# Optimization experiments

Measured on AMD Instinct MI355X. Metric: run time of the kernel, lower is better.

The kernel has to match this reference:

```python
import jax, jax.numpy as jnp
import numpy as np
from jax import lax

EPS = 1e-12  # torch F.normalize eps

DIM = 192
HEADS = 8
B, H, W = 4, 256, 256


def setup_inputs() -> dict:
    key = jax.random.key(0)
    k1, k2, k3, k4 = jax.random.split(key, 4)
    x = jax.random.normal(k1, (B, DIM, H, W), dtype=jnp.float32)
    # 1x1 conv weights stored as [out, in] matrices (kernel size 1)
    qkv_w = jax.random.normal(k2, (DIM * 3, DIM), dtype=jnp.float32) * (1.0 / np.sqrt(DIM))
    # depthwise 3x3 conv, groups = 3*DIM -> OIHW with I=1
    dw_w = jax.random.normal(k3, (DIM * 3, 1, 3, 3), dtype=jnp.float32) * (1.0 / 3.0)
    proj_w = jax.random.normal(k4, (DIM, DIM), dtype=jnp.float32) * (1.0 / np.sqrt(DIM))
    temperature = jnp.ones((HEADS, 1, 1), dtype=jnp.float32)
    return {"x": x, "qkv_w": qkv_w, "dw_w": dw_w, "proj_w": proj_w, "temperature": temperature}


def _l2_normalize(t):
    # matches torch F.normalize(dim=-1): x / max(||x||, eps)
    n = jnp.sqrt(jnp.sum(t * t, axis=-1, keepdims=True))
    return t / jnp.maximum(n, EPS)


def reference(x, qkv_w, dw_w, proj_w, temperature):
    b, c, h, w = x.shape
    heads = temperature.shape[0]
    head_dim = c // heads
    hw = h * w
    # 1x1 conv == per-pixel GEMM
    qkv = jnp.einsum('bchw,oc->bohw', x, qkv_w)
    # depthwise 3x3 conv, padding=1
    qkv = lax.conv_general_dilated(
        qkv, dw_w, window_strides=(1, 1), padding='SAME',
        dimension_numbers=('NCHW', 'OIHW', 'NCHW'),
        feature_group_count=c * 3)
    q, k, v = jnp.split(qkv, 3, axis=1)
    q = _l2_normalize(q.reshape(b, heads, head_dim, hw))
    k = _l2_normalize(k.reshape(b, heads, head_dim, hw))
    v = v.reshape(b, heads, head_dim, hw)
    # tiny [head_dim, head_dim] attention matrix per (b, head)
    attn = jnp.einsum('bhdn,bhen->bhde', q, k) * temperature  # (heads,1,1) broadcasts
    attn = jax.nn.softmax(attn, axis=-1)
    out = jnp.einsum('bhde,bhen->bhdn', attn, v).reshape(b, c, h, w)
    return jnp.einsum('bchw,oc->bohw', out, proj_w)
```

## Files before the change

### kernel.cpp

```cpp
#include <hip/hip_runtime.h>
#include <stdint.h>

typedef unsigned short u16;
typedef short s16x8 __attribute__((ext_vector_type(8)));
typedef float f32x4 __attribute__((ext_vector_type(4)));

#define HW 65536
#define CD 192
#define C3 576
#define QB ((size_t)HW * C3)

static __device__ __forceinline__ float bf2f(u16 u) {
    return __uint_as_float(((uint32_t)u) << 16);
}
static __device__ __forceinline__ u16 f2bf(float f) {
    uint32_t x = __float_as_uint(f);
    return (u16)((x + 0x7fffu + ((x >> 16) & 1u)) >> 16);
}

__launch_bounds__(256)
__global__ void k_convert(const float* __restrict__ in, u16* __restrict__ out, int n4)
{
    int i = blockIdx.x * 256 + threadIdx.x;
    if (i >= n4) return;
    float4 v = ((const float4*)in)[i];
    ushort4 o;
    o.x = f2bf(v.x); o.y = f2bf(v.y); o.z = f2bf(v.z); o.w = f2bf(v.w);
    ((ushort4*)out)[i] = o;
}

__launch_bounds__(256, 2)
__global__ void k_qkv(const u16* __restrict__ A, const float* __restrict__ x,
                      u16* __restrict__ O, int b0)
{
    __shared__ __attribute__((aligned(16))) u16 As[192 * 40];
    __shared__ __attribute__((aligned(16))) u16 Xs[128 * 40];
    const int t    = threadIdx.x;
    const int pb   = blockIdx.z;
    const int m0g  = blockIdx.y * 192;
    const int p0   = blockIdx.x * 128;
    const int lane = t & 63, wid = t >> 6;
    const int quad = lane >> 4, l16 = lane & 15;
    const int wm0  = (wid >> 1) * 96, wn0 = (wid & 1) * 64;

    f32x4 acc[6][4];
    #pragma unroll
    for (int i = 0; i < 6; i++)
        #pragma unroll
        for (int j = 0; j < 4; j++) acc[i][j] = f32x4{0.f, 0.f, 0.f, 0.f};

    const float* Xb = x + (size_t)(b0 + pb) * CD * HW;

    for (int kk = 0; kk < 6; kk++) {
        if (kk) __syncthreads();
        #pragma unroll
        for (int i = 0; i < 3; i++) {
            int s = t + i * 256;
            int m = s >> 2, part = s & 3;
            uint4 v = *(const uint4*)(A + (size_t)(m0g + m) * CD + kk * 32 + part * 8);
            *(uint4*)(&As[m * 40 + part * 8]) = v;
        }
        #pragma unroll
        for (int i = 0; i < 4; i++) {
            int s = t + i * 256;
            int c_l = s >> 5, seg = s & 31;
            float4 v = *(const float4*)(Xb + (size_t)(kk * 32 + c_l) * HW + p0 + seg * 4);
            Xs[(seg * 4 + 0) * 40 + c_l] = f2bf(v.x);
            Xs[(seg * 4 + 1) * 40 + c_l] = f2bf(v.y);
            Xs[(seg * 4 + 2) * 40 + c_l] = f2bf(v.z);
            Xs[(seg * 4 + 3) * 40 + c_l] = f2bf(v.w);
        }
        __syncthreads();
        s16x8 af[6], bfr[4];
        #pragma unroll
        for (int i = 0; i < 6; i++)
            af[i] = *(const s16x8*)(&As[(wm0 + i * 16 + l16) * 40 + quad * 8]);
        #pragma unroll
        for (int j = 0; j < 4; j++)
            bfr[j] = *(const s16x8*)(&Xs[(wn0 + j * 16 + l16) * 40 + quad * 8]);
        #pragma unroll
        for (int i = 0; i < 6; i++)
            #pragma unroll
            for (int j = 0; j < 4; j++)
                acc[i][j] = __builtin_amdgcn_mfma_f32_16x16x32_bf16(af[i], bfr[j], acc[i][j], 0, 0, 0);
    }

    u16* Ob = O + QB * pb;
    #pragma unroll
    for (int i = 0; i < 6; i++) {
        const int o = m0g + wm0 + i * 16 + quad * 4;
        #pragma unroll
        for (int j = 0; j < 4; j++) {
            const int p = p0 + wn0 + j * 16 + l16;
            ushort4 v;
            v.x = f2bf(acc[i][j][0]); v.y = f2bf(acc[i][j][1]);
            v.z = f2bf(acc[i][j][2]); v.w = f2bf(acc[i][j][3]);
            *(ushort4*)(Ob + (size_t)p * C3 + o) = v;
        }
    }
}

#define DW_NB 2304

__launch_bounds__(256, 4)
__global__ void k_dw(const u16* __restrict__ qkv, const float* __restrict__ dww,
                     u16* __restrict__ out, int nbat)
{
    const int cell = blockIdx.x * 256 + threadIdx.x;
    const int slot0 = cell / 144;
    const int cg    = cell - slot0 * 144;
    const int c0    = cg * 4;

    float wf[36];
    #pragma unroll
    for (int i = 0; i < 9; i++)
        *(float4*)&wf[i * 4] = *(const float4*)(dww + cg * 36 + i * 4);

    const int iters = 4 * nbat;
    for (int it = 0; it < iters; it++) {
        const int s  = slot0 + it * 4096;
        const int pb = s >> 14;
        const int p0 = (s & 16383) << 2;
        const int h  = p0 >> 8;
        const int w0 = p0 & 255;

        const u16* src = qkv + (size_t)pb * QB + c0;

        int coff[6]; bool cval[6];
        #pragma unroll
        for (int c = 0; c < 6; c++) {
            int gw  = w0 + c - 1;
            cval[c] = (unsigned)gw < 256u;
            int gwc = gw < 0 ? 0 : (gw > 255 ? 255 : gw);
            coff[c] = gwc * C3;
        }

        uint2 raw[3][6];
        #pragma unroll
        for (int dh = 0; dh < 3; dh++) {
            int gh = h + dh - 1;
            bool rv = (unsigned)gh < 256u;
            int ghc = gh < 0 ? 0 : (gh > 255 ? 255 : gh);
            const u16* rs = src + (size_t)ghc * 256 * C3;
            #pragma unroll
            for (int c = 0; c < 6; c++) {
                uint2 v = *(const uint2*)(rs + coff[c]);
                bool ok = rv && cval[c];
                raw[dh][c].x = ok ? v.x : 0u;
                raw[dh][c].y = ok ? v.y : 0u;
            }
        }

        float acc[4][4];
        #pragma unroll
        for (int px = 0; px < 4; px++)
            #pragma unroll
            for (int j = 0; j < 4; j++) acc[px][j] = 0.f;

        #pragma unroll
        for (int dh = 0; dh < 3; dh++) {
            float v[6][4];
            #pragma unroll
            for (int c = 0; c < 6; c++) {
                const u16* rp = (const u16*)&raw[dh][c];
                #pragma unroll
                for (int j = 0; j < 4; j++) v[c][j] = bf2f(rp[j]);
            }
            #pragma unroll
            for (int dw = 0; dw < 3; dw++) {
                const int k = dh * 3 + dw;
                #pragma unroll
                for (int px = 0; px < 4; px++)
                    #pragma unroll
                    for (int j = 0; j < 4; j++)
                        acc[px][j] += v[px + dw][j] * wf[j * 9 + k];
            }
        }

        u16* dst = out + (size_t)pb * QB + (size_t)p0 * C3 + c0;
        #pragma unroll
        for (int px = 0; px < 4; px++) {
            uint2 o;
            o.x = (uint32_t)f2bf(acc[px][0]) | ((uint32_t)f2bf(acc[px][1]) << 16);
            o.y = (uint32_t)f2bf(acc[px][2]) | ((uint32_t)f2bf(acc[px][3]) << 16);
            *(uint2*)(dst + (size_t)px * C3) = o;
        }
    }
}

#define GNB    16
#define NCHUNK 16

__launch_bounds__(256, 2)
__global__ void k_gram(const u16* __restrict__ dwt, float* __restrict__ gram, int b0)
{
    __shared__ __attribute__((aligned(16))) u16 S[2][48 * 264];
    const int t    = threadIdx.x;
    const int pb   = blockIdx.z, hh = blockIdx.y, blk = blockIdx.x;
    const int lane = t & 63, wid = t >> 6;
    const int quad = lane >> 4, l16 = lane & 15;
    const u16* src = dwt + (size_t)pb * QB + (size_t)blk * (HW / GNB) * C3;
    const int qcol = hh * 24, kcol = CD + hh * 24;
    const int sp_n0 = (t & 127) * 2;
    const int sp_ph = t >> 7;

    f32x4 acc[6];
    #pragma unroll
    for (int i = 0; i < 6; i++) acc[i] = f32x4{0.f, 0.f, 0.f, 0.f};

    uint4 r0[3], r1[3];

    auto stage_load = [&](int cc) {
        const u16* sp = src + (size_t)(cc * 256 + sp_n0) * C3;
        #pragma unroll
        for (int i = 0; i < 3; i++) {
            int part = i * 2 + sp_ph;
            int col  = part < 3 ? qcol + part * 8 : kcol + (part - 3) * 8;
            r0[i] = *(const uint4*)(sp + col);
            r1[i] = *(const uint4*)(sp + C3 + col);
        }
    };
    auto stage_write = [&](int bb) {
        #pragma unroll
        for (int i = 0; i < 3; i++) {
            int part = i * 2 + sp_ph;
            int dstc = part < 3 ? part * 8 : 24 + (part - 3) * 8;
            const u16* a = (const u16*)&r0[i];
            const u16* b = (const u16*)&r1[i];
            #pragma unroll
            for (int w = 0; w < 8; w++) {
                uint32_t d = (uint32_t)a[w] | ((uint32_t)b[w] << 16);
                *(uint32_t*)&S[bb][(dstc + w) * 264 + sp_n0] = d;
            }
        }
    };

    stage_load(0);
    stage_write(0);
    for (int c = 0; c < NCHUNK; c++) {
        const int bb = c & 1;
        __syncthreads();
        if (c + 1 < NCHUNK) stage_load(c + 1);
        #pragma unroll
        for (int kk = 0; kk < 2; kk++) {
            const int k0 = (wid + kk * 4) * 32 + quad * 8;
            s16x8 f0 = *(const s16x8*)&S[bb][( 0 + l16) * 264 + k0];
            s16x8 f1 = *(const s16x8*)&S[bb][(16 + l16) * 264 + k0];
            s16x8 f2 = *(const s16x8*)&S[bb][(32 + l16) * 264 + k0];
            acc[0] = __builtin_amdgcn_mfma_f32_16x16x32_bf16(f0, f0, acc[0], 0, 0, 0);
            acc[1] = __builtin_amdgcn_mfma_f32_16x16x32_bf16(f0, f1, acc[1], 0, 0, 0);
            acc[2] = __builtin_amdgcn_mfma_f32_16x16x32_bf16(f0, f2, acc[2], 0, 0, 0);
            acc[3] = __builtin_amdgcn_mfma_f32_16x16x32_bf16(f1, f1, acc[3], 0, 0, 0);
            acc[4] = __builtin_amdgcn_mfma_f32_16x16x32_bf16(f1, f2, acc[4], 0, 0, 0);
            acc[5] = __builtin_amdgcn_mfma_f32_16x16x32_bf16(f2, f2, acc[5], 0, 0, 0);
        }
        if (c + 1 < NCHUNK) stage_write(bb ^ 1);
    }

    __syncthreads();
    float* red = (float*)&S[0][0];
    #pragma unroll
    for (int tt = 0; tt < 6; tt++)
        #pragma unroll
        for (int r = 0; r < 4; r++)
            red[(wid * 6 + tt) * 256 + (quad * 4 + r) * 16 + l16] = acc[tt][r];
    __syncthreads();
    const int TIr[6] = {0, 0, 0, 1, 1, 2};
    const int TJr[6] = {0, 1, 2, 1, 2, 2};
    float* gb = gram + ((size_t)(b0 + pb) * 8 + hh) * 2304;
    #pragma unroll
    for (int k = 0; k < 6; k++) {
        float s = red[(0 * 6 + k) * 256 + t] + red[(1 * 6 + k) * 256 + t]
                + red[(2 * 6 + k) * 256 + t] + red[(3 * 6 + k) * 256 + t];
        int row = TIr[k] * 16 + (t >> 4);
        int col = TJr[k] * 16 + (t & 15);
        atomicAdd(&gb[row * 48 + col], s);
    }
}

__global__ void k_softmax(const float* __restrict__ gram, const float* __restrict__ temp,
                          float* __restrict__ attnS, int b0)
{
    const int b = b0 + blockIdx.y, hh = blockIdx.x, t = threadIdx.x;
    const float* G = gram + ((size_t)b * 8 + hh) * 2304;
    __shared__ float ksc[24];
    if (t < 24) ksc[t] = 1.f / fmaxf(sqrtf(G[(24 + t) * 48 + 24 + t]), 1e-12f);
    __syncthreads();
    if (t < 24) {
        const float tp = temp[hh];
        const float qs = 1.f / fmaxf(sqrtf(G[t * 48 + t]), 1e-12f);
        const float* row = G + t * 48 + 24;
        float v[24], m = -1e30f;
        #pragma unroll
        for (int e = 0; e < 24; e++) { v[e] = row[e] * qs * ksc[e] * tp; m = fmaxf(m, v[e]); }
        float ssum = 0.f;
        #pragma unroll
        for (int e = 0; e < 24; e++) { v[e] = expf(v[e] - m); ssum += v[e]; }
        const float inv = 1.f / ssum;
        float* orow = attnS + ((size_t)b * 8 + hh) * 576 + t * 24;
        #pragma unroll
        for (int e = 0; e < 24; e++) orow[e] = v[e] * inv;
    }
}

__launch_bounds__(256)
__global__ void k_meff(const float* __restrict__ attnS, const float* __restrict__ projw,
                       u16* __restrict__ meff, int b0, int total)
{
    int g = blockIdx.x * 256 + threadIdx.x;
    if (g >= total) return;
    int b_l = g / 36864, rem = g % 36864;
    int o = rem / CD, c = rem % CD;
    int hh = c / 24, e = c % 24;
    int b = b0 + b_l;
    const float* Arow = attnS + ((size_t)b * 8 + hh) * 576;
    const float* Prow = projw + o * CD + hh * 24;
    float acc = 0.f;
    #pragma unroll
    for (int d = 0; d < 24; d++) acc += Prow[d] * Arow[d * 24 + e];
    meff[(size_t)b * 36864 + o * CD + c] = f2bf(acc);
}

__launch_bounds__(256, 2)
__global__ void k_gemm2(const u16* __restrict__ A, const u16* __restrict__ X,
                        float* __restrict__ O)
{
    __shared__ __attribute__((aligned(16))) u16 As[192 * 40];
    __shared__ __attribute__((aligned(16))) u16 Xs[128 * 40];
    const int t    = threadIdx.x;
    const int pb   = blockIdx.z;
    const int p0   = blockIdx.x * 128;
    const int lane = t & 63, wid = t >> 6;
    const int quad = lane >> 4, l16 = lane & 15;
    const int wm0  = (wid >> 1) * 96, wn0 = (wid & 1) * 64;

    f32x4 acc[6][4];
    #pragma unroll
    for (int i = 0; i < 6; i++)
        #pragma unroll
        for (int j = 0; j < 4; j++) acc[i][j] = f32x4{0.f, 0.f, 0.f, 0.f};

    const u16* Ab = A + (size_t)36864 * pb;
    const u16* Xb = X + QB * pb;

    for (int kk = 0; kk < 6; kk++) {
        if (kk) __syncthreads();
        #pragma unroll
        for (int i = 0; i < 3; i++) {
            int s = t + i * 256;
            int m = s >> 2, part = s & 3;
            uint4 v = *(const uint4*)(Ab + (size_t)m * CD + kk * 32 + part * 8);
            *(uint4*)(&As[m * 40 + part * 8]) = v;
        }
        #pragma unroll
        for (int i = 0; i < 2; i++) {
            int s = t + i * 256;
            int p = s >> 2, part = s & 3;
            uint4 v = *(const uint4*)(Xb + (size_t)(p0 + p) * C3 + 384 + kk * 32 + part * 8);
            *(uint4*)(&Xs[p * 40 + part * 8]) = v;
        }
        __syncthreads();
        s16x8 af[6], bfr[4];
        #pragma unroll
        for (int i = 0; i < 6; i++)
            af[i] = *(const s16x8*)(&As[(wm0 + i * 16 + l16) * 40 + quad * 8]);
        #pragma unroll
        for (int j = 0; j < 4; j++)
            bfr[j] = *(const s16x8*)(&Xs[(wn0 + j * 16 + l16) * 40 + quad * 8]);
        #pragma unroll
        for (int i = 0; i < 6; i++)
            #pragma unroll
            for (int j = 0; j < 4; j++)
                acc[i][j] = __builtin_amdgcn_mfma_f32_16x16x32_bf16(af[i], bfr[j], acc[i][j], 0, 0, 0);
    }

    float* Ob = O + (size_t)CD * HW * pb;
    #pragma unroll
    for (int i = 0; i < 6; i++) {
        const int o = wm0 + i * 16 + quad * 4;
        #pragma unroll
        for (int j = 0; j < 4; j++) {
            const int p = p0 + wn0 + j * 16 + l16;
            #pragma unroll
            for (int r = 0; r < 4; r++)
                Ob[(size_t)(o + r) * HW + p] = acc[i][j][r];
        }
    }
}

extern "C" void kernel_launch(void* const* d_in, const int* in_sizes, int n_in,
                              void* d_out, int out_size, void* d_ws, size_t ws_size,
                              hipStream_t stream)
{
    (void)out_size;
    const float* x     = (const float*)d_in[0];
    const float* qkvw  = (const float*)d_in[1];
    const float* dww   = (const float*)d_in[2];
    const float* projw = (const float*)d_in[3];
    const float* temp  = (const float*)d_in[4];
    for (int i = 0; i < n_in; i++) {
        switch (in_sizes[i]) {
            case 50331648: x     = (const float*)d_in[i]; break;
            case 110592:   qkvw  = (const float*)d_in[i]; break;
            case 5184:     dww   = (const float*)d_in[i]; break;
            case 36864:    projw = (const float*)d_in[i]; break;
            case 8:        temp  = (const float*)d_in[i]; break;
            default: break;
        }
    }
    float* out = (float*)d_out;
    char* ws = (char*)d_ws;

    const size_t gram_off  = 0;
    const size_t asmx_off  = gram_off + 294912;
    const size_t meff_off  = asmx_off + 73728;
    const size_t qkvwb_off = meff_off + 294912;
    const size_t big_off   = (qkvwb_off + 221184 + 255) & ~(size_t)255;

    int P = 4;
    while (P > 1 && big_off + (size_t)P * 2 * QB * 2 > ws_size) P >>= 1;

    float* gram  = (float*)(ws + gram_off);
    float* attnS = (float*)(ws + asmx_off);
    u16*   meff  = (u16*)(ws + meff_off);
    u16*   qkvwb = (u16*)(ws + qkvwb_off);
    u16*   qkvt  = (u16*)(ws + big_off);
    u16*   dwt   = qkvt + (size_t)P * QB;

    hipMemsetAsync(ws + gram_off, 0, 294912, stream);
    k_convert<<<dim3(108), 256, 0, stream>>>(qkvw, qkvwb, 110592 / 4);

    for (int b0 = 0; b0 < 4; b0 += P) {
        k_qkv<<<dim3(512, 3, P), 256, 0, stream>>>(qkvwb, x, qkvt, b0);
        k_dw<<<dim3(DW_NB), 256, 0, stream>>>(qkvt, dww, dwt, P);
        k_gram<<<dim3(GNB, 8, P), 256, 0, stream>>>(dwt, gram, b0);
        k_softmax<<<dim3(8, P), 64, 0, stream>>>(gram, temp, attnS, b0);
        k_meff<<<dim3(P * 144), 256, 0, stream>>>(attnS, projw, meff, b0, P * 36864);
        k_gemm2<<<dim3(512, 1, P), 256, 0, stream>>>(
            meff + (size_t)b0 * 36864, dwt, out + (size_t)b0 * CD * HW);
    }
}
```

Measured before the change: 822.6 us.

## Double-buffer QKV GEMM LDS tiles with register prefetch and packed transposed stores

The QKV 1x1-conv GEMM now uses two LDS buffers, prefetching the next K-slice of weights and activations into registers while MFMAs run on the current slice, so only one barrier per iteration remains. The activation transpose now packs two channels per 32-bit LDS store, and a row stride of 42 is meant to reduce bank conflicts. The cost is double the LDS and extra registers, which may lower occupancy under launch_bounds(256,2). B-fragment reads become four 32-bit loads instead of one 128-bit load.

```diff
diff --git a/kernel.cpp b/kernel.cpp
--- a/kernel.cpp
+++ b/kernel.cpp
@@ -33,8 +33,8 @@
 __global__ void k_qkv(const u16* __restrict__ A, const float* __restrict__ x,
                       u16* __restrict__ O, int b0)
 {
-    __shared__ __attribute__((aligned(16))) u16 As[192 * 40];
-    __shared__ __attribute__((aligned(16))) u16 Xs[128 * 40];
+    __shared__ __attribute__((aligned(16))) u16 As[2][192 * 40];
+    __shared__ __attribute__((aligned(16))) u16 Xs[2][128 * 42];
     const int t    = threadIdx.x;
     const int pb   = blockIdx.z;
     const int m0g  = blockIdx.y * 192;
@@ -42,6 +42,8 @@
     const int lane = t & 63, wid = t >> 6;
     const int quad = lane >> 4, l16 = lane & 15;
     const int wm0  = (wid >> 1) * 96, wn0 = (wid & 1) * 64;
+    const int ch2  = t >> 4;
+    const int px4  = t & 15;
 
     f32x4 acc[6][4];
     #pragma unroll
@@ -49,40 +51,71 @@
         #pragma unroll
         for (int j = 0; j < 4; j++) acc[i][j] = f32x4{0.f, 0.f, 0.f, 0.f};
 
-    const float* Xb = x + (size_t)(b0 + pb) * CD * HW;
-
-    for (int kk = 0; kk < 6; kk++) {
-        if (kk) __syncthreads();
+    const float* Xb = x + (size_t)(b0 + pb) * CD * HW + p0 + px4 * 4;
+
+    float4 xr[2][2];
+    uint4  ar[3];
+
+    auto load_regs = [&](int kk) {
+        #pragma unroll
+        for (int q = 0; q < 2; q++)
+            #pragma unroll
+            for (int e = 0; e < 2; e++)
+                xr[q][e] = *(const float4*)(Xb + (size_t)(kk * 32 + ch2 * 2 + e) * HW + q * 64);
         #pragma unroll
         for (int i = 0; i < 3; i++) {
             int s = t + i * 256;
             int m = s >> 2, part = s & 3;
-            uint4 v = *(const uint4*)(A + (size_t)(m0g + m) * CD + kk * 32 + part * 8);
-            *(uint4*)(&As[m * 40 + part * 8]) = v;
-        }
-        #pragma unroll
-        for (int i = 0; i < 4; i++) {
+            ar[i] = *(const uint4*)(A + (size_t)(m0g + m) * CD + kk * 32 + part * 8);
+        }
+    };
+    auto write_lds = [&](int bb) {
+        #pragma unroll
+        for (int i = 0; i < 3; i++) {
             int s = t + i * 256;
-            int c_l = s >> 5, seg = s & 31;
-            float4 v = *(const float4*)(Xb + (size_t)(kk * 32 + c_l) * HW + p0 + seg * 4);
-            Xs[(seg * 4 + 0) * 40 + c_l] = f2bf(v.x);
-            Xs[(seg * 4 + 1) * 40 + c_l] = f2bf(v.y);
-            Xs[(seg * 4 + 2) * 40 + c_l] = f2bf(v.z);
-            Xs[(seg * 4 + 3) * 40 + c_l] = f2bf(v.w);
-        }
-        __syncthreads();
+            int m = s >> 2, part = s & 3;
+            *(uint4*)(&As[bb][m * 40 + part * 8]) = ar[i];
+        }
+        #pragma unroll
+        for (int q = 0; q < 2; q++) {
+            const float* a0 = (const float*)&xr[q][0];
+            const float* a1 = (const float*)&xr[q][1];
+            #pragma unroll
+            for (int f = 0; f < 4; f++) {
+                uint32_t d = (uint32_t)f2bf(a0[f]) | ((uint32_t)f2bf(a1[f]) << 16);
+                *(uint32_t*)(&Xs[bb][(q * 64 + px4 * 4 + f) * 42 + ch2 * 2]) = d;
+            }
+        }
+    };
+    auto compute = [&](int bb) {
         s16x8 af[6], bfr[4];
         #pragma unroll
         for (int i = 0; i < 6; i++)
-            af[i] = *(const s16x8*)(&As[(wm0 + i * 16 + l16) * 40 + quad * 8]);
-        #pragma unroll
-        for (int j = 0; j < 4; j++)
-            bfr[j] = *(const s16x8*)(&Xs[(wn0 + j * 16 + l16) * 40 + quad * 8]);
+            af[i] = *(const s16x8*)(&As[bb][(wm0 + i * 16 + l16) * 40 + quad * 8]);
+        #pragma unroll
+        for (int j = 0; j < 4; j++) {
+            const uint32_t* qp = (const uint32_t*)(&Xs[bb][(wn0 + j * 16 + l16) * 42 + quad * 8]);
+            union { uint32_t u[4]; s16x8 v; } tmp;
+            tmp.u[0] = qp[0]; tmp.u[1] = qp[1]; tmp.u[2] = qp[2]; tmp.u[3] = qp[3];
+            bfr[j] = tmp.v;
+        }
         #pragma unroll
         for (int i = 0; i < 6; i++)
             #pragma unroll
             for (int j = 0; j < 4; j++)
                 acc[i][j] = __builtin_amdgcn_mfma_f32_16x16x32_bf16(af[i], bfr[j], acc[i][j], 0, 0, 0);
+    };
+
+    load_regs(0);
+    write_lds(0);
+    __syncthreads();
+    for (int kk = 0; kk < 6; kk++) {
+        if (kk < 5) load_regs(kk + 1);
+        compute(kk & 1);
+        if (kk < 5) {
+            write_lds((kk + 1) & 1);
+            __syncthreads();
+        }
     }
 
     u16* Ob = O + QB * pb;
```

Result: slower. 878.8 us (+6.8%).
